# Optimization experiments

Measured on AMD Instinct MI355X. Metric: run time of the kernel, lower is better.

## Reference

```python
import jax, jax.numpy as jnp
import numpy as np

# NF4 codebook (bitsandbytes values)
NF4_LEVELS = jnp.array([-1.0, -0.6961928009986877, -0.5250730514526367, -0.39491748809814453,
                        -0.28444138169288635, -0.18477343022823334, -0.09105003625154495, 0.0,
                        0.07958029955625534, 0.16093020141124725, 0.24611230194568634,
                        0.33791524171829224, 0.44070982933044434, 0.5626170039176941,
                        0.7229568362236023, 1.0], dtype=jnp.float32)

IN_FEATURES = 4096
OUT_FEATURES = 4096


def setup_inputs() -> dict:
    key = jax.random.key(0)
    k1, k2, k3, k4 = jax.random.split(key, 4)
    x = jax.random.normal(k1, (4, 2048, IN_FEATURES), dtype=jnp.float32)
    # packed uint8 bytes (stored as int32 in [0,256)), shape (O, I//2)
    packed = jax.random.randint(k2, (OUT_FEATURES, IN_FEATURES // 2), 0, 256, dtype=jnp.int32)
    absmax = jax.random.uniform(k3, (OUT_FEATURES,), dtype=jnp.float32) + 1e-3
    bias = jax.random.normal(k4, (OUT_FEATURES,), dtype=jnp.float32)
    return {"x": x, "packed": packed, "absmax": absmax, "bias": bias}


def dequantize_nf4(packed, absmax):
    # packed: (O, I//2) int bytes; high nibble first, then low nibble
    high = (packed >> 4) & 15
    low = packed & 15
    idx = jnp.stack([high, low], axis=2).reshape(packed.shape[0], -1)  # (O, I)
    w = NF4_LEVELS[idx]                    # LUT dequant, (O, I)
    return w * absmax[:, None]             # per-row absmax scaling


def reference(x, packed, absmax, bias):
    # forward: dequantize weight on-the-fly, then F.linear(x, W, bias)
    w = dequantize_nf4(packed, absmax)     # (O, I)
    return jnp.einsum('bsi,oi->bso', x, w) + bias
```

## Files before the change

### kernel.cpp

```cpp
#include <hip/hip_runtime.h>
#include <hip/hip_bf16.h>
#include <stdint.h>

#define M_DIM 8192
#define N_DIM 4096
#define K_DIM 4096

typedef __bf16 bf16_t;
typedef __attribute__((ext_vector_type(8))) __bf16 bf16x8;
typedef __attribute__((ext_vector_type(4))) __bf16 bf16x4;
typedef __attribute__((ext_vector_type(4))) float f32x4;

__constant__ float NF4_LUT[16] = {
    -1.0f, -0.6961928009986877f, -0.5250730514526367f, -0.39491748809814453f,
    -0.28444138169288635f, -0.18477343022823334f, -0.09105003625154495f, 0.0f,
    0.07958029955625534f, 0.16093020141124725f, 0.24611230194568634f,
    0.33791524171829224f, 0.44070982933044434f, 0.5626170039176941f,
    0.7229568362236023f, 1.0f};

__global__ __launch_bounds__(256) void dequant_nf4_kernel(
    const int* __restrict__ packed, const float* __restrict__ absmax,
    bf16_t* __restrict__ W) {
  const int t = blockIdx.x * 256 + threadIdx.x;
  const int row = t >> 9;
  const int c = t & 511;
  const int lane = threadIdx.x & 63;
  const int lutbits = __float_as_int(NF4_LUT[lane & 15]);

  const int4 p = ((const int4*)packed)[t];
  const float am = absmax[row];
  bf16x8 v;
#pragma unroll
  for (int q = 0; q < 4; ++q) {
    const int byte = (q == 0 ? p.x : q == 1 ? p.y : q == 2 ? p.z : p.w) & 255;
    const float hi =
        __int_as_float(__builtin_amdgcn_ds_bpermute(((byte >> 4) & 15) << 2, lutbits));
    const float lo =
        __int_as_float(__builtin_amdgcn_ds_bpermute((byte & 15) << 2, lutbits));
    v[2 * q] = (bf16_t)(hi * am);
    v[2 * q + 1] = (bf16_t)(lo * am);
  }
  *((bf16x8*)&W[(size_t)row * K_DIM + c * 8]) = v;
}

__global__ __launch_bounds__(256) void cvt_bf16_kernel(
    const float* __restrict__ x, bf16_t* __restrict__ y) {
  const int t = blockIdx.x * 256 + threadIdx.x;
  const float4 a = ((const float4*)x)[t];
  bf16x4 v;
  v[0] = (bf16_t)a.x; v[1] = (bf16_t)a.y; v[2] = (bf16_t)a.z; v[3] = (bf16_t)a.w;
  *((bf16x4*)&y[(size_t)t * 4]) = v;
}

#define GLD_LDS16(g, l)                                                     \
  __builtin_amdgcn_global_load_lds(                                        \
      (const __attribute__((address_space(1))) void*)(g),                   \
      (__attribute__((address_space(3))) void*)(l), 16, 0, 0)

#define MFMA_BF16(a, b, c) \
  __builtin_amdgcn_mfma_f32_16x16x32_bf16((a), (b), (c), 0, 0, 0)

#define STAGE_A1(tt, lds)                                    \
  do {                                                       \
    GLD_LDS16(gA1a + (size_t)(tt) * 64, (lds) + dA0);        \
    GLD_LDS16(gA1b + (size_t)(tt) * 64, (lds) + dA0 + 16384);\
  } while (0)
#define STAGE_A2(tt, lds)                                    \
  do {                                                       \
    GLD_LDS16(gA2a + (size_t)(tt) * 64, (lds) + dA0 + 8192); \
    GLD_LDS16(gA2b + (size_t)(tt) * 64, (lds) + dA0 + 24576);\
  } while (0)
#define STAGE_B1(tt, lds)                                    \
  do {                                                       \
    GLD_LDS16(gB1a + (size_t)(tt) * 64, (lds) + dB0);        \
    GLD_LDS16(gB1b + (size_t)(tt) * 64, (lds) + dB0 + 16384);\
  } while (0)
#define STAGE_B2(tt, lds)                                    \
  do {                                                       \
    GLD_LDS16(gB2a + (size_t)(tt) * 64, (lds) + dB0 + 4096); \
    GLD_LDS16(gB2b + (size_t)(tt) * 64, (lds) + dB0 + 20480);\
  } while (0)

#define END_BARRIER()                \
  asm volatile("" ::: "memory");     \
  __builtin_amdgcn_s_barrier();      \
  asm volatile("" ::: "memory")

#define MID_BARRIER()                                   \
  asm volatile("" ::: "memory");                        \
  __builtin_amdgcn_s_barrier();                         \
  asm volatile("s_waitcnt lgkmcnt(0)" ::: "memory");    \
  __builtin_amdgcn_sched_barrier(0)

__global__ __launch_bounds__(512, 2) void gemm_nf4_kernel(
    const bf16_t* __restrict__ A, const bf16_t* __restrict__ B,
    const float* __restrict__ bias, float* __restrict__ C) {
  constexpr int NT = K_DIM / 64;
  __shared__ __align__(16) bf16_t sA[2][256 * 64];
  __shared__ __align__(16) bf16_t sB[2][256 * 64];

  const int tid = threadIdx.x;
  const int wave = tid >> 6, lane = tid & 63;
  const int wm = wave >> 2, wn = wave & 3;
  const int quad = lane >> 4, l15 = lane & 15, l7 = lane & 7;

  const int id = (blockIdx.x & 7) * 64 + (blockIdx.x >> 3);
  const int blockM = (id & 31) * 256;
  const int blockN = (id >> 5) * 256;

  const int rqa = tid >> 3;
  const int cira = ((tid & 7) ^ (rqa & 7)) * 8;
  const bf16_t* gA1a = A + (size_t)(blockM + rqa) * K_DIM + cira;
  const bf16_t* gA1b = gA1a + (size_t)128 * K_DIM;
  const bf16_t* gA2a = gA1a + (size_t)64 * K_DIM;
  const bf16_t* gA2b = gA1a + (size_t)192 * K_DIM;
  const int s0 = tid >> 8, cis = tid & 255;
  const int rqb = cis >> 3;
  const int cirb = ((cis & 7) ^ (rqb & 7)) * 8;
  const bf16_t* gB1a = B + (size_t)(blockN + s0 * 64 + rqb) * K_DIM + cirb;
  const bf16_t* gB1b = gB1a + (size_t)128 * K_DIM;
  const bf16_t* gB2a = gB1a + (size_t)32 * K_DIM;
  const bf16_t* gB2b = gB1a + (size_t)160 * K_DIM;
  const int dA0 = tid * 16;
  const int dB0 = s0 * 8192 + cis * 16;

  const int aRd0 = wm * 16384 + l15 * 128 + ((quad ^ l7) * 16);
  const int aRd1 = wm * 16384 + l15 * 128 + (((4 | quad) ^ l7) * 16);
  const int bRd0 = wn * 8192 + l15 * 128 + ((quad ^ l7) * 16);
  const int bRd1 = wn * 8192 + l15 * 128 + (((4 | quad) ^ l7) * 16);

  f32x4 acc[8][4];
#pragma unroll
  for (int i = 0; i < 8; ++i)
#pragma unroll
    for (int j = 0; j < 4; ++j) acc[i][j] = (f32x4)(0.0f);

  {
    char* sa0 = (char*)sA[0];
    char* sb0 = (char*)sB[0];
    char* sa1 = (char*)sA[1];
    char* sb1 = (char*)sB[1];
    STAGE_A1(0, sa0);
    STAGE_B1(0, sb0);
    STAGE_A2(0, sa0);
    STAGE_B2(0, sb0);
    STAGE_A1(1, sa1);
    STAGE_B1(1, sb1);
    asm volatile("s_waitcnt vmcnt(4)" ::: "memory");
    __builtin_amdgcn_s_barrier();
    asm volatile("" ::: "memory");
  }

  for (int t = 0; t < NT; ++t) {
    char* sa = (char*)sA[t & 1];
    char* sao = (char*)sA[(t + 1) & 1];
    char* sb = (char*)sB[t & 1];
    char* sbo = (char*)sB[(t + 1) & 1];

    bf16x8 af[4][2], bq[2][2];

#pragma unroll
    for (int i = 0; i < 4; ++i) {
      af[i][0] = *(const bf16x8*)(sa + aRd0 + i * 2048);
      af[i][1] = *(const bf16x8*)(sa + aRd1 + i * 2048);
    }
#pragma unroll
    for (int j = 0; j < 2; ++j) {
      bq[j][0] = *(const bf16x8*)(sb + bRd0 + j * 2048);
      bq[j][1] = *(const bf16x8*)(sb + bRd1 + j * 2048);
    }
    if (t + 1 < NT) STAGE_A2(t + 1, sao);
    asm volatile("s_waitcnt lgkmcnt(8)" ::: "memory");
    MID_BARRIER();
    __builtin_amdgcn_s_setprio(1);
#pragma unroll
    for (int i = 0; i < 4; ++i)
#pragma unroll
      for (int j = 0; j < 2; ++j) {
        acc[i][j] = MFMA_BF16(af[i][0], bq[j][0], acc[i][j]);
        acc[i][j] = MFMA_BF16(af[i][1], bq[j][1], acc[i][j]);
      }
    __builtin_amdgcn_s_setprio(0);
    END_BARRIER();

#pragma unroll
    for (int j = 0; j < 2; ++j) {
      bq[j][0] = *(const bf16x8*)(sb + bRd0 + (2 + j) * 2048);
      bq[j][1] = *(const bf16x8*)(sb + bRd1 + (2 + j) * 2048);
    }
    if (t + 1 < NT) STAGE_B2(t + 1, sbo);
    MID_BARRIER();
    __builtin_amdgcn_s_setprio(1);
#pragma unroll
    for (int i = 0; i < 4; ++i)
#pragma unroll
      for (int j = 0; j < 2; ++j) {
        acc[i][2 + j] = MFMA_BF16(af[i][0], bq[j][0], acc[i][2 + j]);
        acc[i][2 + j] = MFMA_BF16(af[i][1], bq[j][1], acc[i][2 + j]);
      }
    __builtin_amdgcn_s_setprio(0);
    END_BARRIER();

#pragma unroll
    for (int i = 0; i < 4; ++i) {
      af[i][0] = *(const bf16x8*)(sa + aRd0 + (4 + i) * 2048);
      af[i][1] = *(const bf16x8*)(sa + aRd1 + (4 + i) * 2048);
    }
#pragma unroll
    for (int j = 0; j < 2; ++j) {
      bq[j][0] = *(const bf16x8*)(sb + bRd0 + j * 2048);
      bq[j][1] = *(const bf16x8*)(sb + bRd1 + j * 2048);
    }
    if (t + 2 < NT) STAGE_A1(t + 2, sa);
    asm volatile("s_waitcnt lgkmcnt(8)" ::: "memory");
    MID_BARRIER();
    __builtin_amdgcn_s_setprio(1);
#pragma unroll
    for (int i = 0; i < 4; ++i)
#pragma unroll
      for (int j = 0; j < 2; ++j) {
        acc[4 + i][j] = MFMA_BF16(af[i][0], bq[j][0], acc[4 + i][j]);
        acc[4 + i][j] = MFMA_BF16(af[i][1], bq[j][1], acc[4 + i][j]);
      }
    __builtin_amdgcn_s_setprio(0);
    END_BARRIER();

#pragma unroll
    for (int j = 0; j < 2; ++j) {
      bq[j][0] = *(const bf16x8*)(sb + bRd0 + (2 + j) * 2048);
      bq[j][1] = *(const bf16x8*)(sb + bRd1 + (2 + j) * 2048);
    }
    if (t + 2 < NT) STAGE_B1(t + 2, sb);
    MID_BARRIER();
    __builtin_amdgcn_s_setprio(1);
#pragma unroll
    for (int i = 0; i < 4; ++i)
#pragma unroll
      for (int j = 0; j < 2; ++j) {
        acc[4 + i][2 + j] = MFMA_BF16(af[i][0], bq[j][0], acc[4 + i][2 + j]);
        acc[4 + i][2 + j] = MFMA_BF16(af[i][1], bq[j][1], acc[4 + i][2 + j]);
      }
    __builtin_amdgcn_s_setprio(0);
    if (t < NT - 2)
      asm volatile("s_waitcnt vmcnt(4)" ::: "memory");
    else
      asm volatile("s_waitcnt vmcnt(0)" ::: "memory");
    END_BARRIER();
  }

#pragma unroll
  for (int nf = 0; nf < 4; ++nf) {
    const int n = blockN + wn * 64 + nf * 16 + l15;
    const float bv = bias[n];
#pragma unroll
    for (int mf = 0; mf < 8; ++mf) {
      const int m0 = blockM + wm * 128 + mf * 16 + quad * 4;
      f32x4 v = acc[mf][nf];
      C[(size_t)(m0 + 0) * N_DIM + n] = v[0] + bv;
      C[(size_t)(m0 + 1) * N_DIM + n] = v[1] + bv;
      C[(size_t)(m0 + 2) * N_DIM + n] = v[2] + bv;
      C[(size_t)(m0 + 3) * N_DIM + n] = v[3] + bv;
    }
  }
}

__global__ __launch_bounds__(256) void fallback_kernel(
    const float* __restrict__ x, const int* __restrict__ packed,
    const float* __restrict__ absmax, const float* __restrict__ bias,
    float* __restrict__ out) {
  const int idx = blockIdx.x * 256 + threadIdx.x;
  const int m = idx / N_DIM, n = idx % N_DIM;
  const int* prow = packed + (size_t)n * (K_DIM / 2);
  const float* xr = x + (size_t)m * K_DIM;
  float s = 0.0f;
  for (int p = 0; p < K_DIM / 2; ++p) {
    const int b = prow[p] & 255;
    s += xr[2 * p] * NF4_LUT[(b >> 4) & 15] + xr[2 * p + 1] * NF4_LUT[b & 15];
  }
  out[idx] = s * absmax[n] + bias[n];
}

extern "C" void kernel_launch(void* const* d_in, const int* in_sizes, int n_in,
                              void* d_out, int out_size, void* d_ws,
                              size_t ws_size, hipStream_t stream) {
  const float* x = (const float*)d_in[0];
  const int* packed = (const int*)d_in[1];
  const float* absmax = (const float*)d_in[2];
  const float* bias = (const float*)d_in[3];
  float* out = (float*)d_out;

  const size_t wBytes = (size_t)N_DIM * K_DIM * sizeof(bf16_t);
  const size_t xBytes = (size_t)M_DIM * K_DIM * sizeof(bf16_t);
  if (ws_size < wBytes + xBytes) {
    fallback_kernel<<<dim3((M_DIM * N_DIM) / 256), dim3(256), 0, stream>>>(
        x, packed, absmax, bias, out);
    return;
  }

  bf16_t* W = (bf16_t*)d_ws;
  bf16_t* xb = (bf16_t*)((char*)d_ws + wBytes);

  dequant_nf4_kernel<<<dim3((N_DIM * (K_DIM / 2) / 4) / 256), dim3(256), 0,
                       stream>>>(packed, absmax, W);
  cvt_bf16_kernel<<<dim3((M_DIM * K_DIM / 4) / 256), dim3(256), 0, stream>>>(
      x, xb);
  gemm_nf4_kernel<<<dim3((M_DIM / 256) * (N_DIM / 256)), dim3(512), 0,
                    stream>>>(xb, W, bias, out);
}
```

Measured before the change: 527.9 us.

## Switch GEMM inner loop to 32x32x16 bf16 MFMA with fewer phases

Replaces the 16x16x32 MFMA tiling with 32x32x16 MFMA, where each wave computes 4x2 32x32 output tiles as f32x16 accumulators. The per-iteration schedule shrinks from four LDS-read/MFMA phases to two, with the A and B stage loads issued together. Larger MFMA tiles cut LDS fragment reads per flop and barrier count, at the cost of coarser overlap between loads and compute and a different epilogue store pattern.

```diff
diff --git a/kernel.cpp b/kernel.cpp
--- a/kernel.cpp
+++ b/kernel.cpp
@@ -10,6 +10,7 @@
 typedef __attribute__((ext_vector_type(8))) __bf16 bf16x8;
 typedef __attribute__((ext_vector_type(4))) __bf16 bf16x4;
 typedef __attribute__((ext_vector_type(4))) float f32x4;
+typedef __attribute__((ext_vector_type(16))) float f32x16;
 
 __constant__ float NF4_LUT[16] = {
     -1.0f, -0.6961928009986877f, -0.5250730514526367f, -0.39491748809814453f,
@@ -57,8 +58,8 @@
       (const __attribute__((address_space(1))) void*)(g),                   \
       (__attribute__((address_space(3))) void*)(l), 16, 0, 0)
 
-#define MFMA_BF16(a, b, c) \
-  __builtin_amdgcn_mfma_f32_16x16x32_bf16((a), (b), (c), 0, 0, 0)
+#define MFMA32(a, b, c) \
+  __builtin_amdgcn_mfma_f32_32x32x16_bf16((a), (b), (c), 0, 0, 0)
 
 #define STAGE_A1(tt, lds)                                    \
   do {                                                       \
@@ -102,7 +103,7 @@
   const int tid = threadIdx.x;
   const int wave = tid >> 6, lane = tid & 63;
   const int wm = wave >> 2, wn = wave & 3;
-  const int quad = lane >> 4, l15 = lane & 15, l7 = lane & 7;
+  const int l31 = lane & 31, hi = lane >> 5, l7 = lane & 7;
 
   const int id = (blockIdx.x & 7) * 64 + (blockIdx.x >> 3);
   const int blockM = (id & 31) * 256;
@@ -124,16 +125,17 @@
   const int dA0 = tid * 16;
   const int dB0 = s0 * 8192 + cis * 16;
 
-  const int aRd0 = wm * 16384 + l15 * 128 + ((quad ^ l7) * 16);
-  const int aRd1 = wm * 16384 + l15 * 128 + (((4 | quad) ^ l7) * 16);
-  const int bRd0 = wn * 8192 + l15 * 128 + ((quad ^ l7) * 16);
-  const int bRd1 = wn * 8192 + l15 * 128 + (((4 | quad) ^ l7) * 16);
-
-  f32x4 acc[8][4];
-#pragma unroll
-  for (int i = 0; i < 8; ++i)
-#pragma unroll
-    for (int j = 0; j < 4; ++j) acc[i][j] = (f32x4)(0.0f);
+  const int aBase = (wm * 128 + l31) * 128;
+  const int bBase = (wn * 64 + l31) * 128;
+  int cOff[4];
+#pragma unroll
+  for (int ks = 0; ks < 4; ++ks) cOff[ks] = ((ks * 2 + hi) ^ l7) * 16;
+
+  f32x16 acc[4][2];
+#pragma unroll
+  for (int i = 0; i < 4; ++i)
+#pragma unroll
+    for (int j = 0; j < 2; ++j) acc[i][j] = (f32x16)(0.0f);
 
   {
     char* sa0 = (char*)sA[0];
@@ -157,89 +159,53 @@
     char* sb = (char*)sB[t & 1];
     char* sbo = (char*)sB[(t + 1) & 1];
 
-    bf16x8 af[4][2], bq[2][2];
-
-#pragma unroll
-    for (int i = 0; i < 4; ++i) {
-      af[i][0] = *(const bf16x8*)(sa + aRd0 + i * 2048);
-      af[i][1] = *(const bf16x8*)(sa + aRd1 + i * 2048);
+    bf16x8 af[2][4], bq[2][4];
+
+#pragma unroll
+    for (int mt = 0; mt < 2; ++mt)
+#pragma unroll
+      for (int ks = 0; ks < 4; ++ks)
+        af[mt][ks] = *(const bf16x8*)(sa + aBase + mt * 4096 + cOff[ks]);
+#pragma unroll
+    for (int nt = 0; nt < 2; ++nt)
+#pragma unroll
+      for (int ks = 0; ks < 4; ++ks)
+        bq[nt][ks] = *(const bf16x8*)(sb + bBase + nt * 4096 + cOff[ks]);
+    if (t + 1 < NT) {
+      STAGE_A2(t + 1, sao);
+      STAGE_B2(t + 1, sbo);
     }
-#pragma unroll
-    for (int j = 0; j < 2; ++j) {
-      bq[j][0] = *(const bf16x8*)(sb + bRd0 + j * 2048);
-      bq[j][1] = *(const bf16x8*)(sb + bRd1 + j * 2048);
-    }
-    if (t + 1 < NT) STAGE_A2(t + 1, sao);
     asm volatile("s_waitcnt lgkmcnt(8)" ::: "memory");
     MID_BARRIER();
     __builtin_amdgcn_s_setprio(1);
 #pragma unroll
-    for (int i = 0; i < 4; ++i)
-#pragma unroll
-      for (int j = 0; j < 2; ++j) {
-        acc[i][j] = MFMA_BF16(af[i][0], bq[j][0], acc[i][j]);
-        acc[i][j] = MFMA_BF16(af[i][1], bq[j][1], acc[i][j]);
-      }
+    for (int ks = 0; ks < 4; ++ks)
+#pragma unroll
+      for (int mt = 0; mt < 2; ++mt)
+#pragma unroll
+        for (int nt = 0; nt < 2; ++nt)
+          acc[mt][nt] = MFMA32(af[mt][ks], bq[nt][ks], acc[mt][nt]);
     __builtin_amdgcn_s_setprio(0);
     END_BARRIER();
 
 #pragma unroll
-    for (int j = 0; j < 2; ++j) {
-      bq[j][0] = *(const bf16x8*)(sb + bRd0 + (2 + j) * 2048);
-      bq[j][1] = *(const bf16x8*)(sb + bRd1 + (2 + j) * 2048);
+    for (int mt = 0; mt < 2; ++mt)
+#pragma unroll
+      for (int ks = 0; ks < 4; ++ks)
+        af[mt][ks] = *(const bf16x8*)(sa + aBase + 8192 + mt * 4096 + cOff[ks]);
+    if (t + 2 < NT) {
+      STAGE_A1(t + 2, sa);
+      STAGE_B1(t + 2, sb);
     }
-    if (t + 1 < NT) STAGE_B2(t + 1, sbo);
     MID_BARRIER();
     __builtin_amdgcn_s_setprio(1);
 #pragma unroll
-    for (int i = 0; i < 4; ++i)
-#pragma unroll
-      for (int j = 0; j < 2; ++j) {
-        acc[i][2 + j] = MFMA_BF16(af[i][0], bq[j][0], acc[i][2 + j]);
-        acc[i][2 + j] = MFMA_BF16(af[i][1], bq[j][1], acc[i][2 + j]);
-      }
-    __builtin_amdgcn_s_setprio(0);
-    END_BARRIER();
-
-#pragma unroll
-    for (int i = 0; i < 4; ++i) {
-      af[i][0] = *(const bf16x8*)(sa + aRd0 + (4 + i) * 2048);
-      af[i][1] = *(const bf16x8*)(sa + aRd1 + (4 + i) * 2048);
-    }
-#pragma unroll
-    for (int j = 0; j < 2; ++j) {
-      bq[j][0] = *(const bf16x8*)(sb + bRd0 + j * 2048);
-      bq[j][1] = *(const bf16x8*)(sb + bRd1 + j * 2048);
-    }
-    if (t + 2 < NT) STAGE_A1(t + 2, sa);
-    asm volatile("s_waitcnt lgkmcnt(8)" ::: "memory");
-    MID_BARRIER();
-    __builtin_amdgcn_s_setprio(1);
-#pragma unroll
-    for (int i = 0; i < 4; ++i)
-#pragma unroll
-      for (int j = 0; j < 2; ++j) {
-        acc[4 + i][j] = MFMA_BF16(af[i][0], bq[j][0], acc[4 + i][j]);
-        acc[4 + i][j] = MFMA_BF16(af[i][1], bq[j][1], acc[4 + i][j]);
-      }
-    __builtin_amdgcn_s_setprio(0);
-    END_BARRIER();
-
-#pragma unroll
-    for (int j = 0; j < 2; ++j) {
-      bq[j][0] = *(const bf16x8*)(sb + bRd0 + (2 + j) * 2048);
-      bq[j][1] = *(const bf16x8*)(sb + bRd1 + (2 + j) * 2048);
-    }
-    if (t + 2 < NT) STAGE_B1(t + 2, sb);
-    MID_BARRIER();
-    __builtin_amdgcn_s_setprio(1);
-#pragma unroll
-    for (int i = 0; i < 4; ++i)
-#pragma unroll
-      for (int j = 0; j < 2; ++j) {
-        acc[4 + i][2 + j] = MFMA_BF16(af[i][0], bq[j][0], acc[4 + i][2 + j]);
-        acc[4 + i][2 + j] = MFMA_BF16(af[i][1], bq[j][1], acc[4 + i][2 + j]);
-      }
+    for (int ks = 0; ks < 4; ++ks)
+#pragma unroll
+      for (int mt = 0; mt < 2; ++mt)
+#pragma unroll
+        for (int nt = 0; nt < 2; ++nt)
+          acc[2 + mt][nt] = MFMA32(af[mt][ks], bq[nt][ks], acc[2 + mt][nt]);
     __builtin_amdgcn_s_setprio(0);
     if (t < NT - 2)
       asm volatile("s_waitcnt vmcnt(4)" ::: "memory");
@@ -249,17 +215,18 @@
   }
 
 #pragma unroll
-  for (int nf = 0; nf < 4; ++nf) {
-    const int n = blockN + wn * 64 + nf * 16 + l15;
+  for (int nt = 0; nt < 2; ++nt) {
+    const int n = blockN + wn * 64 + nt * 32 + l31;
     const float bv = bias[n];
 #pragma unroll
-    for (int mf = 0; mf < 8; ++mf) {
-      const int m0 = blockM + wm * 128 + mf * 16 + quad * 4;
-      f32x4 v = acc[mf][nf];
-      C[(size_t)(m0 + 0) * N_DIM + n] = v[0] + bv;
-      C[(size_t)(m0 + 1) * N_DIM + n] = v[1] + bv;
-      C[(size_t)(m0 + 2) * N_DIM + n] = v[2] + bv;
-      C[(size_t)(m0 + 3) * N_DIM + n] = v[3] + bv;
+    for (int mt = 0; mt < 4; ++mt) {
+      const int mbase = blockM + wm * 128 + mt * 32 + hi * 4;
+      f32x16 v = acc[mt][nt];
+#pragma unroll
+      for (int r = 0; r < 16; ++r) {
+        const int m = mbase + (r & 3) + 8 * (r >> 2);
+        C[(size_t)m * N_DIM + n] = v[r] + bv;
+      }
     }
   }
 }
```

New measurement: 521.4 us. Within noise of the previous version (-1.2%).
